# Kernel optimization log

Measured on AMD Instinct MI355X. Metric: run time of the kernel, lower is better.

Reference implementation:

```python
import jax, jax.numpy as jnp
import numpy as np

B, HM_C, H, W = 8, 2, 152, 272
EMB = 128
KOBJ = 128
KGATHER = 8192
NID = (500, 300)
HM_WEIGHT, WH_WEIGHT, OFF_WEIGHT = 1.0, 0.1, 1.0


def setup_inputs() -> dict:
    key = jax.random.key(0)
    ks = jax.random.split(key, 16)
    hm_pred = jax.random.normal(ks[0], (B, HM_C, H, W), jnp.float32)
    wh_pred = jax.random.normal(ks[1], (B, 2, H, W), jnp.float32)
    reg_pred = jax.random.normal(ks[2], (B, 2, H, W), jnp.float32)
    id_pred = jax.random.normal(ks[3], (B, EMB, H, W), jnp.float32)
    ind = jax.random.randint(ks[4], (B, KOBJ), 0, H * W, jnp.int32)
    cls_obj = jax.random.randint(ks[5], (B, KOBJ), 0, HM_C, jnp.int32)
    # gaussian-ish heatmap in [0,1) with exact 1.0 at object centers
    hm = jax.random.uniform(ks[6], (B, HM_C, H, W), jnp.float32) ** 4
    bidx = jnp.arange(B)[:, None]
    hm = hm.reshape(B, HM_C, H * W).at[bidx, cls_obj, ind].set(1.0).reshape(B, HM_C, H, W)
    wh = jax.random.uniform(ks[7], (B, KOBJ, 2), jnp.float32) * 50.0
    reg = jax.random.uniform(ks[8], (B, KOBJ, 2), jnp.float32)
    reg_mask = (jax.random.uniform(ks[9], (B, KOBJ)) < 0.5).astype(jnp.float32)
    u = jax.random.uniform(ks[10], (B, 1, H, W))
    cmap = jax.random.randint(ks[11], (B, 1, H, W), 0, HM_C, jnp.int32)
    cls_id_map = jnp.where(u < 0.01, cmap, -1).astype(jnp.int32)
    cls_tr_ids = jnp.stack([
        jax.random.randint(ks[12], (B, H, W), 0, NID[0], jnp.int32),
        jax.random.randint(ks[13], (B, H, W), 0, NID[1], jnp.int32)], axis=1)
    W0 = jax.random.normal(ks[14], (NID[0], EMB), jnp.float32) * 0.01
    b0 = jnp.zeros((NID[0],), jnp.float32)
    W1 = jax.random.normal(ks[15], (NID[1], EMB), jnp.float32) * 0.01
    b1 = jnp.zeros((NID[1],), jnp.float32)
    s_det = jnp.full((1,), -1.85, jnp.float32)
    s_id = jnp.full((1,), -1.05, jnp.float32)
    return dict(hm_pred=hm_pred, wh_pred=wh_pred, reg_pred=reg_pred, id_pred=id_pred,
                hm=hm, wh=wh, reg=reg, reg_mask=reg_mask, ind=ind,
                cls_id_map=cls_id_map, cls_tr_ids=cls_tr_ids,
                W0=W0, b0=b0, W1=W1, b1=b1, s_det=s_det, s_id=s_id)


def _sigmoid(x):
    return jnp.clip(jax.nn.sigmoid(x), 1e-4, 1.0 - 1e-4)


def focal_loss(pred, gt):
    pos = gt == 1.0
    neg_w = (1.0 - gt) ** 4
    pos_loss = jnp.where(pos, jnp.log(pred) * (1.0 - pred) ** 2, 0.0).sum()
    neg_loss = jnp.where(pos, 0.0, jnp.log(1.0 - pred) * pred ** 2 * neg_w).sum()
    num_pos = pos.sum().astype(pred.dtype)
    return jnp.where(num_pos > 0, -(pos_loss + neg_loss) / jnp.maximum(num_pos, 1.0), -neg_loss)


def gather_feat(feat, ind):  # feat [B,C,H,W], ind [B,K] -> [B,K,C]
    b, c, h, w = feat.shape
    f = feat.reshape(b, c, h * w)
    idx = jnp.broadcast_to(ind[:, None, :], (b, c, ind.shape[1]))
    return jnp.take_along_axis(f, idx, axis=2).transpose(0, 2, 1)


def reg_l1_loss(output, mask, ind, target):
    pred = gather_feat(output, ind)            # [B,K,C]
    m = mask[:, :, None]                       # expanded mask
    c = pred.shape[-1]
    num = jnp.abs(pred * m - target * m).sum()
    return num / (mask.sum() * c + 1e-4)


def reid_class_loss(id_pred, cls_id_map, cls_tr_ids, cls_id, Wc, bc, nid):
    mask = (cls_id_map[:, 0] == cls_id).reshape(-1)              # [B*H*W]
    cnt = mask.sum()
    idx = jnp.nonzero(mask, size=KGATHER, fill_value=0)[0]       # static-size gather
    valid = jnp.arange(KGATHER) < cnt
    feat = id_pred.transpose(0, 2, 3, 1).reshape(-1, EMB)[idx]   # [K,EMB]
    norm = jnp.maximum(jnp.linalg.norm(feat, axis=1, keepdims=True), 1e-12)
    emb_scale = np.float32(np.sqrt(2.0) * np.log(nid - 1.0))
    emb = emb_scale * feat / norm
    logits = emb @ Wc.T + bc                                     # [K,nid]
    tgt = cls_tr_ids[:, cls_id].reshape(-1)[idx]
    tgt = jnp.where(valid, tgt, -1)                              # padded -> ignore_index
    logp = jax.nn.log_softmax(logits, axis=-1)
    nll = jnp.where(tgt >= 0,
                    -jnp.take_along_axis(logp, jnp.clip(tgt, 0)[:, None], axis=1)[:, 0], 0.0)
    n_valid = (tgt >= 0).sum().astype(logits.dtype)
    ce = nll.sum() / jnp.maximum(n_valid, 1.0)                   # CE mean over non-ignored
    term = ce / jnp.maximum(cnt.astype(logits.dtype), 1.0)       # / nelement()
    return jnp.where(cnt > 0, term, 0.0)


def reference(hm_pred, wh_pred, reg_pred, id_pred, hm, wh, reg, reg_mask, ind,
              cls_id_map, cls_tr_ids, W0, b0, W1, b1, s_det, s_id):
    hm_loss = focal_loss(_sigmoid(hm_pred), hm)
    wh_loss = reg_l1_loss(wh_pred, reg_mask, ind, wh)
    off_loss = reg_l1_loss(reg_pred, reg_mask, ind, reg)
    reid_loss = (reid_class_loss(id_pred, cls_id_map, cls_tr_ids, 0, W0, b0, NID[0])
                 + reid_class_loss(id_pred, cls_id_map, cls_tr_ids, 1, W1, b1, NID[1]))
    det_loss = HM_WEIGHT * hm_loss + WH_WEIGHT * wh_loss + OFF_WEIGHT * off_loss
    loss = 0.5 * (jnp.exp(-s_det[0]) * det_loss + jnp.exp(-s_id[0]) * reid_loss
                  + s_det[0] + s_id[0])
    return loss, hm_loss, wh_loss, off_loss, reid_loss
```

## Files before the change

### kernel.cpp

```cpp
#include <hip/hip_runtime.h>
#include <math.h>

#define BB    8
#define HMC   2
#define HW    41344
#define EMBD  128
#define KOBJ  128
#define KG    8192
#define NID0  500
#define NID1  300
#define TE    16


__device__ __forceinline__ float wave_sum(float v) {
    #pragma unroll
    for (int o = 32; o > 0; o >>= 1) v += __shfl_down(v, o, 64);
    return v;
}

__global__ void fused1_kernel(const float4* __restrict__ hp,
                              const float4* __restrict__ gt,
                              const int4*   __restrict__ cmap,
                              const float*  __restrict__ wh_pred,
                              const float*  __restrict__ reg_pred,
                              const float*  __restrict__ wh,
                              const float*  __restrict__ reg,
                              const float*  __restrict__ mask,
                              const int*    __restrict__ ind,
                              float* __restrict__ wsf, int n4, int nc4) {
    int* wsi = (int*)wsf;
    int tid = threadIdx.x;
    int gid = blockIdx.x * blockDim.x + tid;
    int gstride = gridDim.x * blockDim.x;

    __shared__ int stage0[1024], stage1[1024];
    __shared__ int lcnt0, lcnt1, gbase0, gbase1;
    __shared__ float sm[3][4];

    if (tid == 0) { lcnt0 = 0; lcnt1 = 0; }
    __syncthreads();

    for (int i = gid; i < nc4; i += gstride) {
        int4 v = cmap[i];
        int b4 = i * 4;
        if (v.x == 0) stage0[atomicAdd(&lcnt0,1)] = b4+0; else if (v.x == 1) stage1[atomicAdd(&lcnt1,1)] = b4+0;
        if (v.y == 0) stage0[atomicAdd(&lcnt0,1)] = b4+1; else if (v.y == 1) stage1[atomicAdd(&lcnt1,1)] = b4+1;
        if (v.z == 0) stage0[atomicAdd(&lcnt0,1)] = b4+2; else if (v.z == 1) stage1[atomicAdd(&lcnt1,1)] = b4+2;
        if (v.w == 0) stage0[atomicAdd(&lcnt0,1)] = b4+3; else if (v.w == 1) stage1[atomicAdd(&lcnt1,1)] = b4+3;
    }
    __syncthreads();
    if (tid == 0) gbase0 = (lcnt0 > 0) ? atomicAdd(wsi + 8, lcnt0) : 0;
    if (tid == 1) gbase1 = (lcnt1 > 0) ? atomicAdd(wsi + 9, lcnt1) : 0;
    __syncthreads();
    for (int j = tid; j < lcnt0; j += blockDim.x) { int q = gbase0 + j; if (q < KG) wsi[16 + q] = stage0[j]; }
    for (int j = tid; j < lcnt1; j += blockDim.x) { int q = gbase1 + j; if (q < KG) wsi[16 + KG + q] = stage1[j]; }

    float pos = 0.f, neg = 0.f, cnt = 0.f;
    for (int i = gid; i < n4; i += gstride) {
        float4 x = hp[i];
        float4 g = gt[i];
        float xs[4] = {x.x, x.y, x.z, x.w};
        float gs[4] = {g.x, g.y, g.z, g.w};
        #pragma unroll
        for (int j = 0; j < 4; ++j) {
            float s = 1.f / (1.f + expf(-xs[j]));
            s = fminf(fmaxf(s, 1e-4f), 1.f - 1e-4f);
            float gv = gs[j];
            if (gv == 1.f) {
                float om = 1.f - s;
                pos += logf(s) * om * om;
                cnt += 1.f;
            } else {
                float nw = 1.f - gv; nw = nw * nw; nw = nw * nw;
                neg += logf(1.f - s) * s * s * nw;
            }
        }
    }
    {
        float a = wave_sum(pos), b = wave_sum(neg), c = wave_sum(cnt);
        int lane = tid & 63, wid = tid >> 6;
        if (lane == 0) { sm[0][wid] = a; sm[1][wid] = b; sm[2][wid] = c; }
        __syncthreads();
        if (tid == 0) {
            float s0 = 0, s1 = 0, s2 = 0;
            #pragma unroll
            for (int w = 0; w < 4; ++w) { s0 += sm[0][w]; s1 += sm[1][w]; s2 += sm[2][w]; }
            atomicAdd(wsf + 0, s0);
            atomicAdd(wsf + 1, s1);
            atomicAdd(wsf + 2, s2);
        }
    }

    if (blockIdx.x == 0) {
        __syncthreads();
        float nwh = 0.f, noff = 0.f, msum = 0.f;
        for (int t = tid; t < BB * KOBJ; t += blockDim.x) {
            int b = t / KOBJ;
            float m = mask[t];
            int id = ind[t];
            const float* wp = wh_pred + (size_t)b * 2 * HW;
            const float* rp = reg_pred + (size_t)b * 2 * HW;
            float p0 = wp[id], p1 = wp[HW + id];
            float q0 = rp[id], q1 = rp[HW + id];
            float t0 = wh[t * 2], t1 = wh[t * 2 + 1];
            float r0 = reg[t * 2], r1 = reg[t * 2 + 1];
            nwh  += fabsf(p0 * m - t0 * m) + fabsf(p1 * m - t1 * m);
            noff += fabsf(q0 * m - r0 * m) + fabsf(q1 * m - r1 * m);
            msum += m;
        }
        float a = wave_sum(nwh), b = wave_sum(noff), c = wave_sum(msum);
        int lane = tid & 63, wid = tid >> 6;
        if (lane == 0) { sm[0][wid] = a; sm[1][wid] = b; sm[2][wid] = c; }
        __syncthreads();
        if (tid == 0) {
            float s0 = 0, s1 = 0, s2 = 0;
            #pragma unroll
            for (int w = 0; w < 4; ++w) { s0 += sm[0][w]; s1 += sm[1][w]; s2 += sm[2][w]; }
            wsf[3] = s0; wsf[4] = s1; wsf[5] = s2;
        }
    }
}

__global__ void gather_kernel(const float* __restrict__ id_pred,
                              const int*   __restrict__ cls_tr,
                              float* __restrict__ wsf,
                              float esc0, float esc1) {
    int cls = blockIdx.y;
    int* wsi = (int*)wsf;
    int cnt = wsi[8 + cls];
    int m = cnt < KG ? cnt : KG;
    const int* idxArr = wsi + 16 + cls * KG;
    int* tgtArr = wsi + 16 + 2 * KG + cls * KG;
    float* embArr = wsf + 16 + 4 * KG + (size_t)cls * KG * EMBD;
    float escale = cls ? esc1 : esc0;
    __shared__ float red[2];
    int tid = threadIdx.x;
    for (int i = blockIdx.x; i < m; i += gridDim.x) {
        int p = idxArr[i];
        int b = p / HW, hw = p - b * HW;
        float f = id_pred[((size_t)b * EMBD + tid) * HW + hw];
        float ss = f * f;
        #pragma unroll
        for (int o = 32; o > 0; o >>= 1) ss += __shfl_down(ss, o, 64);
        if ((tid & 63) == 0) red[tid >> 6] = ss;
        __syncthreads();
        float s = red[0] + red[1];
        float scale = escale / fmaxf(sqrtf(s), 1e-12f);
        embArr[(size_t)i * EMBD + tid] = f * scale;
        if (tid == 0) tgtArr[i] = cls_tr[((size_t)b * 2 + cls) * HW + hw];
        __syncthreads();
    }
}

__device__ void final_combine(const float* wsf, float nll0, float nll1,
                              int c0, int c1,
                              const float* sdet, const float* sid,
                              float* out) {
    float pos = wsf[0], neg = wsf[1], npos = wsf[2];
    float hm_loss = (npos > 0.f) ? -(pos + neg) / fmaxf(npos, 1.f) : -neg;
    float wh_loss  = wsf[3] / (wsf[5] * 2.f + 1e-4f);
    float off_loss = wsf[4] / (wsf[5] * 2.f + 1e-4f);
    float reid = 0.f;
    if (c0 > 0) {
        float nv = (float)(c0 < KG ? c0 : KG);
        reid += (nll0 / fmaxf(nv, 1.f)) / fmaxf((float)c0, 1.f);
    }
    if (c1 > 0) {
        float nv = (float)(c1 < KG ? c1 : KG);
        reid += (nll1 / fmaxf(nv, 1.f)) / fmaxf((float)c1, 1.f);
    }
    float det = hm_loss + 0.1f * wh_loss + off_loss;
    float sd = sdet[0], si = sid[0];
    out[0] = 0.5f * (expf(-sd) * det + expf(-si) * reid + sd + si);
    out[1] = hm_loss;
    out[2] = wh_loss;
    out[3] = off_loss;
    out[4] = reid;
}

__global__ __launch_bounds__(256)
void reid_logits_kernel(const float* __restrict__ W0, const float* __restrict__ b0,
                        const float* __restrict__ W1, const float* __restrict__ b1,
                        const float* __restrict__ sdet, const float* __restrict__ sid,
                        float* __restrict__ wsf, float* __restrict__ out) {
    int* wsi = (int*)wsf;
    int cls = blockIdx.y;
    int tid = threadIdx.x;

    int c0full = wsi[8], c1full = wsi[9];
    int m0 = c0full < KG ? c0full : KG;
    int m1 = c1full < KG ? c1full : KG;
    int a0 = (m0 + TE - 1) / TE, a1 = (m1 + TE - 1) / TE;
    int nact = a0 + a1;

    if (nact == 0) {
        if (blockIdx.x == 0 && cls == 0 && tid == 0)
            final_combine(wsf, 0.f, 0.f, c0full, c1full, sdet, sid, out);
        return;
    }
    int m = cls ? m1 : m0;
    int base = blockIdx.x * TE;
    if (base >= m) return;
    int nval = m - base; if (nval > TE) nval = TE;

    int nid = cls ? NID1 : NID0;
    const float* Wc = cls ? W1 : W0;
    const float* bc = cls ? b1 : b0;
    const float* embArr = wsf + 16 + 4 * KG + (size_t)cls * KG * EMBD;
    const int*   tgtArr = wsi + 16 + 2 * KG + cls * KG;

    __shared__ float emb_s[TE][EMBD];
    __shared__ int   tgt_s[TE];
    __shared__ float tgtl_s[TE];
    __shared__ float red_m[TE][4];
    __shared__ float red_s[TE][4];

    {
        const float4* src = (const float4*)(embArr + (size_t)base * EMBD);
        float4* dst = (float4*)&emb_s[0][0];
        int lim = nval * (EMBD / 4);
        for (int j = tid; j < TE * (EMBD / 4); j += 256)
            dst[j] = (j < lim) ? src[j] : make_float4(0.f, 0.f, 0.f, 0.f);
    }
    if (tid < TE) { tgt_s[tid] = (tid < nval) ? tgtArr[base + tid] : -1; tgtl_s[tid] = 0.f; }
    __syncthreads();

    int r0 = tid, r1 = tid + 256;
    bool v1ok = r1 < nid;
    const float4* wr0 = (const float4*)(Wc + (size_t)r0 * EMBD);
    const float4* wr1 = (const float4*)(Wc + (size_t)(v1ok ? r1 : 0) * EMBD);

    float acc0[TE], acc1[TE];
    #pragma unroll
    for (int e = 0; e < TE; ++e) { acc0[e] = 0.f; acc1[e] = 0.f; }

    for (int j = 0; j < EMBD / 4; ++j) {
        float4 w0 = wr0[j];
        float4 w1 = wr1[j];
        #pragma unroll
        for (int e = 0; e < TE; ++e) {
            float4 em = ((const float4*)emb_s[e])[j];
            acc0[e] = fmaf(w0.x, em.x, fmaf(w0.y, em.y, fmaf(w0.z, em.z, fmaf(w0.w, em.w, acc0[e]))));
            acc1[e] = fmaf(w1.x, em.x, fmaf(w1.y, em.y, fmaf(w1.z, em.z, fmaf(w1.w, em.w, acc1[e]))));
        }
    }
    float bias0 = bc[r0];
    float bias1 = v1ok ? bc[r1] : 0.f;
    #pragma unroll
    for (int e = 0; e < TE; ++e) {
        acc0[e] += bias0;
        acc1[e] = v1ok ? (acc1[e] + bias1) : -1e30f;
        if (r0 == tgt_s[e]) tgtl_s[e] = acc0[e];
        if (v1ok && r1 == tgt_s[e]) tgtl_s[e] = acc1[e];
    }

    int lane = tid & 63, wid = tid >> 6;

    float mx[TE];
    #pragma unroll
    for (int e = 0; e < TE; ++e) mx[e] = fmaxf(acc0[e], acc1[e]);
    #pragma unroll
    for (int o = 32; o > 0; o >>= 1) {
        #pragma unroll
        for (int e = 0; e < TE; ++e) mx[e] = fmaxf(mx[e], __shfl_xor(mx[e], o, 64));
    }
    if (lane == 0) {
        #pragma unroll
        for (int e = 0; e < TE; ++e) red_m[e][wid] = mx[e];
    }
    __syncthreads();
    float bm[TE];
    #pragma unroll
    for (int e = 0; e < TE; ++e)
        bm[e] = fmaxf(fmaxf(red_m[e][0], red_m[e][1]), fmaxf(red_m[e][2], red_m[e][3]));

    float se[TE];
    #pragma unroll
    for (int e = 0; e < TE; ++e) se[e] = expf(acc0[e] - bm[e]) + expf(acc1[e] - bm[e]);
    #pragma unroll
    for (int o = 32; o > 0; o >>= 1) {
        #pragma unroll
        for (int e = 0; e < TE; ++e) se[e] += __shfl_xor(se[e], o, 64);
    }
    if (lane == 0) {
        #pragma unroll
        for (int e = 0; e < TE; ++e) red_s[e][wid] = se[e];
    }
    __syncthreads();

    if (tid == 0) {
        float nll = 0.f;
        #pragma unroll
        for (int e = 0; e < TE; ++e) {
            if (e < nval) {
                float S = red_s[e][0] + red_s[e][1] + red_s[e][2] + red_s[e][3];
                nll += bm[e] + logf(S) - tgtl_s[e];
            }
        }
        atomicAdd(wsf + 6 + cls, nll);
        __threadfence();
        int old = atomicAdd(wsi + 10, 1);
        if (old == nact - 1) {
            float nll0 = atomicAdd(wsf + 6, 0.f);
            float nll1 = atomicAdd(wsf + 7, 0.f);
            final_combine(wsf, nll0, nll1, c0full, c1full, sdet, sid, out);
        }
    }
}

extern "C" void kernel_launch(void* const* d_in, const int* in_sizes, int n_in,
                              void* d_out, int out_size, void* d_ws, size_t ws_size,
                              hipStream_t stream) {
    const float* hm_pred   = (const float*)d_in[0];
    const float* wh_pred   = (const float*)d_in[1];
    const float* reg_pred  = (const float*)d_in[2];
    const float* id_pred   = (const float*)d_in[3];
    const float* hm        = (const float*)d_in[4];
    const float* wh        = (const float*)d_in[5];
    const float* reg       = (const float*)d_in[6];
    const float* reg_mask  = (const float*)d_in[7];
    const int*   ind       = (const int*)d_in[8];
    const int*   cls_map   = (const int*)d_in[9];
    const int*   cls_tr    = (const int*)d_in[10];
    const float* W0        = (const float*)d_in[11];
    const float* b0        = (const float*)d_in[12];
    const float* W1        = (const float*)d_in[13];
    const float* b1        = (const float*)d_in[14];
    const float* s_det     = (const float*)d_in[15];
    const float* s_id      = (const float*)d_in[16];

    float* wsf = (float*)d_ws;

    hipMemsetAsync(d_ws, 0, 64, stream);

    const int n4  = (BB * HMC * HW) / 4;
    const int nc4 = (BB * HW) / 4;

    fused1_kernel<<<512, 256, 0, stream>>>(
        (const float4*)hm_pred, (const float4*)hm, (const int4*)cls_map,
        wh_pred, reg_pred, wh, reg, reg_mask, ind, wsf, n4, nc4);

    const float esc0 = (float)(sqrt(2.0) * log((double)NID0 - 1.0));
    const float esc1 = (float)(sqrt(2.0) * log((double)NID1 - 1.0));

    gather_kernel<<<dim3(1024, 2), 128, 0, stream>>>(id_pred, cls_tr, wsf, esc0, esc1);

    reid_logits_kernel<<<dim3(KG / TE, 2), 256, 0, stream>>>(
        W0, b0, W1, b1, s_det, s_id, wsf, (float*)d_out);
}
```

Baseline: 87.12 us.

## Fuse three kernels into one persistent kernel with a grid barrier

```diff
diff --git a/kernel.cpp b/kernel.cpp
--- a/kernel.cpp
+++ b/kernel.cpp
@@ -10,6 +10,7 @@
 #define NID0  500
 #define NID1  300
 #define TE    16
+#define GRID  512
 
 
 __device__ __forceinline__ float wave_sum(float v) {
@@ -17,25 +18,64 @@
     for (int o = 32; o > 0; o >>= 1) v += __shfl_down(v, o, 64);
     return v;
 }
-
-__global__ void fused1_kernel(const float4* __restrict__ hp,
-                              const float4* __restrict__ gt,
-                              const int4*   __restrict__ cmap,
-                              const float*  __restrict__ wh_pred,
-                              const float*  __restrict__ reg_pred,
-                              const float*  __restrict__ wh,
-                              const float*  __restrict__ reg,
-                              const float*  __restrict__ mask,
-                              const int*    __restrict__ ind,
-                              float* __restrict__ wsf, int n4, int nc4) {
+__device__ __forceinline__ float aread_f(float* p) { return atomicAdd(p, 0.0f); }
+__device__ __forceinline__ int   aread_i(int* p)   { return atomicAdd(p, 0); }
+
+__device__ void final_combine(float* wsf, int c0, int c1,
+                              const float* sdet, const float* sid,
+                              float* out) {
+    int* wsi = (int*)wsf;
+    (void)wsi;
+    float pos  = aread_f(wsf + 0), neg = aread_f(wsf + 1), npos = aread_f(wsf + 2);
+    float swh  = aread_f(wsf + 3), soff = aread_f(wsf + 4), msum = aread_f(wsf + 5);
+    float nll0 = aread_f(wsf + 6), nll1 = aread_f(wsf + 7);
+    float hm_loss = (npos > 0.f) ? -(pos + neg) / fmaxf(npos, 1.f) : -neg;
+    float wh_loss  = swh  / (msum * 2.f + 1e-4f);
+    float off_loss = soff / (msum * 2.f + 1e-4f);
+    float reid = 0.f;
+    if (c0 > 0) {
+        float nv = (float)(c0 < KG ? c0 : KG);
+        reid += (nll0 / fmaxf(nv, 1.f)) / fmaxf((float)c0, 1.f);
+    }
+    if (c1 > 0) {
+        float nv = (float)(c1 < KG ? c1 : KG);
+        reid += (nll1 / fmaxf(nv, 1.f)) / fmaxf((float)c1, 1.f);
+    }
+    float det = hm_loss + 0.1f * wh_loss + off_loss;
+    float sd = sdet[0], si = sid[0];
+    out[0] = 0.5f * (__expf(-sd) * det + __expf(-si) * reid + sd + si);
+    out[1] = hm_loss;
+    out[2] = wh_loss;
+    out[3] = off_loss;
+    out[4] = reid;
+}
+
+__global__ __launch_bounds__(256, 2)
+void mega_kernel(const float4* __restrict__ hp, const float4* __restrict__ gt,
+                 const int4* __restrict__ cmap,
+                 const float* __restrict__ wh_pred, const float* __restrict__ reg_pred,
+                 const float* __restrict__ wh, const float* __restrict__ reg,
+                 const float* __restrict__ mask, const int* __restrict__ ind,
+                 const float* __restrict__ id_pred, const int* __restrict__ cls_tr,
+                 const float* __restrict__ W0, const float* __restrict__ b0,
+                 const float* __restrict__ W1, const float* __restrict__ b1,
+                 const float* __restrict__ sdet, const float* __restrict__ sid,
+                 float* __restrict__ wsf, float* __restrict__ out,
+                 float esc0, float esc1, int n4, int nc4)
+{
     int* wsi = (int*)wsf;
     int tid = threadIdx.x;
-    int gid = blockIdx.x * blockDim.x + tid;
-    int gstride = gridDim.x * blockDim.x;
+    int gid = blockIdx.x * 256 + tid;
+    const int gstride = GRID * 256;
 
     __shared__ int stage0[1024], stage1[1024];
     __shared__ int lcnt0, lcnt1, gbase0, gbase1;
     __shared__ float sm[3][4];
+    __shared__ float emb_s[TE][EMBD];
+    __shared__ int   tgt_s[TE];
+    __shared__ float tgtl_s[TE];
+    __shared__ float red_m[TE][4];
+    __shared__ float red_s[TE][4];
 
     if (tid == 0) { lcnt0 = 0; lcnt1 = 0; }
     __syncthreads();
@@ -52,31 +92,31 @@
     if (tid == 0) gbase0 = (lcnt0 > 0) ? atomicAdd(wsi + 8, lcnt0) : 0;
     if (tid == 1) gbase1 = (lcnt1 > 0) ? atomicAdd(wsi + 9, lcnt1) : 0;
     __syncthreads();
-    for (int j = tid; j < lcnt0; j += blockDim.x) { int q = gbase0 + j; if (q < KG) wsi[16 + q] = stage0[j]; }
-    for (int j = tid; j < lcnt1; j += blockDim.x) { int q = gbase1 + j; if (q < KG) wsi[16 + KG + q] = stage1[j]; }
-
-    float pos = 0.f, neg = 0.f, cnt = 0.f;
-    for (int i = gid; i < n4; i += gstride) {
-        float4 x = hp[i];
-        float4 g = gt[i];
-        float xs[4] = {x.x, x.y, x.z, x.w};
-        float gs[4] = {g.x, g.y, g.z, g.w};
-        #pragma unroll
-        for (int j = 0; j < 4; ++j) {
-            float s = 1.f / (1.f + expf(-xs[j]));
-            s = fminf(fmaxf(s, 1e-4f), 1.f - 1e-4f);
-            float gv = gs[j];
-            if (gv == 1.f) {
-                float om = 1.f - s;
-                pos += logf(s) * om * om;
-                cnt += 1.f;
-            } else {
-                float nw = 1.f - gv; nw = nw * nw; nw = nw * nw;
-                neg += logf(1.f - s) * s * s * nw;
+    for (int j = tid; j < lcnt0; j += 256) { int q = gbase0 + j; if (q < KG) wsi[16 + q] = stage0[j]; }
+    for (int j = tid; j < lcnt1; j += 256) { int q = gbase1 + j; if (q < KG) wsi[16 + KG + q] = stage1[j]; }
+
+    {
+        float pos = 0.f, neg = 0.f, cnt = 0.f;
+        for (int i = gid; i < n4; i += gstride) {
+            float4 x = hp[i];
+            float4 g = gt[i];
+            float xs[4] = {x.x, x.y, x.z, x.w};
+            float gs[4] = {g.x, g.y, g.z, g.w};
+            #pragma unroll
+            for (int j = 0; j < 4; ++j) {
+                float s = 1.f / (1.f + __expf(-xs[j]));
+                s = fminf(fmaxf(s, 1e-4f), 1.f - 1e-4f);
+                float gv = gs[j];
+                if (gv == 1.f) {
+                    float om = 1.f - s;
+                    pos += __logf(s) * om * om;
+                    cnt += 1.f;
+                } else {
+                    float nw = 1.f - gv; nw = nw * nw; nw = nw * nw;
+                    neg += __logf(1.f - s) * s * s * nw;
+                }
             }
         }
-    }
-    {
         float a = wave_sum(pos), b = wave_sum(neg), c = wave_sum(cnt);
         int lane = tid & 63, wid = tid >> 6;
         if (lane == 0) { sm[0][wid] = a; sm[1][wid] = b; sm[2][wid] = c; }
@@ -94,7 +134,7 @@
     if (blockIdx.x == 0) {
         __syncthreads();
         float nwh = 0.f, noff = 0.f, msum = 0.f;
-        for (int t = tid; t < BB * KOBJ; t += blockDim.x) {
+        for (int t = tid; t < BB * KOBJ; t += 256) {
             int b = t / KOBJ;
             float m = mask[t];
             int id = ind[t];
@@ -116,113 +156,82 @@
             float s0 = 0, s1 = 0, s2 = 0;
             #pragma unroll
             for (int w = 0; w < 4; ++w) { s0 += sm[0][w]; s1 += sm[1][w]; s2 += sm[2][w]; }
-            wsf[3] = s0; wsf[4] = s1; wsf[5] = s2;
-        }
-    }
-}
-
-__global__ void gather_kernel(const float* __restrict__ id_pred,
-                              const int*   __restrict__ cls_tr,
-                              float* __restrict__ wsf,
-                              float esc0, float esc1) {
-    int cls = blockIdx.y;
-    int* wsi = (int*)wsf;
-    int cnt = wsi[8 + cls];
-    int m = cnt < KG ? cnt : KG;
-    const int* idxArr = wsi + 16 + cls * KG;
-    int* tgtArr = wsi + 16 + 2 * KG + cls * KG;
-    float* embArr = wsf + 16 + 4 * KG + (size_t)cls * KG * EMBD;
-    float escale = cls ? esc1 : esc0;
-    __shared__ float red[2];
-    int tid = threadIdx.x;
-    for (int i = blockIdx.x; i < m; i += gridDim.x) {
-        int p = idxArr[i];
-        int b = p / HW, hw = p - b * HW;
-        float f = id_pred[((size_t)b * EMBD + tid) * HW + hw];
-        float ss = f * f;
-        #pragma unroll
-        for (int o = 32; o > 0; o >>= 1) ss += __shfl_down(ss, o, 64);
-        if ((tid & 63) == 0) red[tid >> 6] = ss;
-        __syncthreads();
-        float s = red[0] + red[1];
-        float scale = escale / fmaxf(sqrtf(s), 1e-12f);
-        embArr[(size_t)i * EMBD + tid] = f * scale;
-        if (tid == 0) tgtArr[i] = cls_tr[((size_t)b * 2 + cls) * HW + hw];
-        __syncthreads();
-    }
-}
-
-__device__ void final_combine(const float* wsf, float nll0, float nll1,
-                              int c0, int c1,
-                              const float* sdet, const float* sid,
-                              float* out) {
-    float pos = wsf[0], neg = wsf[1], npos = wsf[2];
-    float hm_loss = (npos > 0.f) ? -(pos + neg) / fmaxf(npos, 1.f) : -neg;
-    float wh_loss  = wsf[3] / (wsf[5] * 2.f + 1e-4f);
-    float off_loss = wsf[4] / (wsf[5] * 2.f + 1e-4f);
-    float reid = 0.f;
-    if (c0 > 0) {
-        float nv = (float)(c0 < KG ? c0 : KG);
-        reid += (nll0 / fmaxf(nv, 1.f)) / fmaxf((float)c0, 1.f);
-    }
-    if (c1 > 0) {
-        float nv = (float)(c1 < KG ? c1 : KG);
-        reid += (nll1 / fmaxf(nv, 1.f)) / fmaxf((float)c1, 1.f);
-    }
-    float det = hm_loss + 0.1f * wh_loss + off_loss;
-    float sd = sdet[0], si = sid[0];
-    out[0] = 0.5f * (expf(-sd) * det + expf(-si) * reid + sd + si);
-    out[1] = hm_loss;
-    out[2] = wh_loss;
-    out[3] = off_loss;
-    out[4] = reid;
-}
-
-__global__ __launch_bounds__(256)
-void reid_logits_kernel(const float* __restrict__ W0, const float* __restrict__ b0,
-                        const float* __restrict__ W1, const float* __restrict__ b1,
-                        const float* __restrict__ sdet, const float* __restrict__ sid,
-                        float* __restrict__ wsf, float* __restrict__ out) {
-    int* wsi = (int*)wsf;
-    int cls = blockIdx.y;
-    int tid = threadIdx.x;
-
-    int c0full = wsi[8], c1full = wsi[9];
+            atomicAdd(wsf + 3, s0);
+            atomicAdd(wsf + 4, s1);
+            atomicAdd(wsf + 5, s2);
+        }
+    }
+
+    __threadfence();
+    __syncthreads();
+    if (tid == 0) {
+        atomicAdd(wsi + 11, 1);
+        while (aread_i(wsi + 11) < GRID) __builtin_amdgcn_s_sleep(8);
+    }
+    __syncthreads();
+
+    int c0full = aread_i(wsi + 8);
+    int c1full = aread_i(wsi + 9);
     int m0 = c0full < KG ? c0full : KG;
     int m1 = c1full < KG ? c1full : KG;
     int a0 = (m0 + TE - 1) / TE, a1 = (m1 + TE - 1) / TE;
     int nact = a0 + a1;
 
     if (nact == 0) {
-        if (blockIdx.x == 0 && cls == 0 && tid == 0)
-            final_combine(wsf, 0.f, 0.f, c0full, c1full, sdet, sid, out);
+        if (blockIdx.x == 0 && tid == 0)
+            final_combine(wsf, c0full, c1full, sdet, sid, out);
         return;
     }
-    int m = cls ? m1 : m0;
-    int base = blockIdx.x * TE;
-    if (base >= m) return;
+    int t = blockIdx.x;
+    if (t >= nact) return;
+    int cls  = (t < a0) ? 0 : 1;
+    int tile = (t < a0) ? t : t - a0;
+    int m    = cls ? m1 : m0;
+    int base = tile * TE;
     int nval = m - base; if (nval > TE) nval = TE;
 
     int nid = cls ? NID1 : NID0;
     const float* Wc = cls ? W1 : W0;
     const float* bc = cls ? b1 : b0;
-    const float* embArr = wsf + 16 + 4 * KG + (size_t)cls * KG * EMBD;
-    const int*   tgtArr = wsi + 16 + 2 * KG + cls * KG;
-
-    __shared__ float emb_s[TE][EMBD];
-    __shared__ int   tgt_s[TE];
-    __shared__ float tgtl_s[TE];
-    __shared__ float red_m[TE][4];
-    __shared__ float red_s[TE][4];
+    int* idxArr = wsi + 16 + cls * KG;
+    float escale = cls ? esc1 : esc0;
 
     {
-        const float4* src = (const float4*)(embArr + (size_t)base * EMBD);
-        float4* dst = (float4*)&emb_s[0][0];
-        int lim = nval * (EMBD / 4);
-        for (int j = tid; j < TE * (EMBD / 4); j += 256)
-            dst[j] = (j < lim) ? src[j] : make_float4(0.f, 0.f, 0.f, 0.f);
-    }
-    if (tid < TE) { tgt_s[tid] = (tid < nval) ? tgtArr[base + tid] : -1; tgtl_s[tid] = 0.f; }
+        int e  = tid >> 4;
+        int cg = tid & 15;
+        if (e < nval) {
+            int p = aread_i(idxArr + base + e);
+            int b = p / HW, hw = p - b * HW;
+            const float* src = id_pred + (size_t)b * EMBD * HW + hw;
+            float f[8];
+            float ss = 0.f;
+            #pragma unroll
+            for (int j = 0; j < 8; ++j) {
+                f[j] = src[(size_t)(cg * 8 + j) * HW];
+                ss += f[j] * f[j];
+            }
+            #pragma unroll
+            for (int o = 1; o < 16; o <<= 1) ss += __shfl_xor(ss, o, 64);
+            float scale = escale / fmaxf(__builtin_sqrtf(ss), 1e-12f);
+            float4* dst = (float4*)&emb_s[e][cg * 8];
+            dst[0] = make_float4(f[0]*scale, f[1]*scale, f[2]*scale, f[3]*scale);
+            dst[1] = make_float4(f[4]*scale, f[5]*scale, f[6]*scale, f[7]*scale);
+        } else {
+            float4* dst = (float4*)&emb_s[e][cg * 8];
+            dst[0] = make_float4(0.f, 0.f, 0.f, 0.f);
+            dst[1] = make_float4(0.f, 0.f, 0.f, 0.f);
+        }
+        if (tid < TE) {
+            int tg = -1;
+            if (tid < nval) {
+                int p = aread_i(idxArr + base + tid);
+                int b = p / HW, hw = p - b * HW;
+                tg = cls_tr[((size_t)b * 2 + cls) * HW + hw];
+            }
+            tgt_s[tid] = tg;
+            tgtl_s[tid] = 0.f;
+        }
+    }
     __syncthreads();
 
     int r0 = tid, r1 = tid + 256;
@@ -276,7 +285,7 @@
 
     float se[TE];
     #pragma unroll
-    for (int e = 0; e < TE; ++e) se[e] = expf(acc0[e] - bm[e]) + expf(acc1[e] - bm[e]);
+    for (int e = 0; e < TE; ++e) se[e] = __expf(acc0[e] - bm[e]) + __expf(acc1[e] - bm[e]);
     #pragma unroll
     for (int o = 32; o > 0; o >>= 1) {
         #pragma unroll
@@ -294,17 +303,14 @@
         for (int e = 0; e < TE; ++e) {
             if (e < nval) {
                 float S = red_s[e][0] + red_s[e][1] + red_s[e][2] + red_s[e][3];
-                nll += bm[e] + logf(S) - tgtl_s[e];
+                nll += bm[e] + __logf(S) - tgtl_s[e];
             }
         }
         atomicAdd(wsf + 6 + cls, nll);
         __threadfence();
         int old = atomicAdd(wsi + 10, 1);
-        if (old == nact - 1) {
-            float nll0 = atomicAdd(wsf + 6, 0.f);
-            float nll1 = atomicAdd(wsf + 7, 0.f);
-            final_combine(wsf, nll0, nll1, c0full, c1full, sdet, sid, out);
-        }
+        if (old == nact - 1)
+            final_combine(wsf, c0full, c1full, sdet, sid, out);
     }
 }
 
@@ -335,16 +341,12 @@
 
     const int n4  = (BB * HMC * HW) / 4;
     const int nc4 = (BB * HW) / 4;
-
-    fused1_kernel<<<512, 256, 0, stream>>>(
-        (const float4*)hm_pred, (const float4*)hm, (const int4*)cls_map,
-        wh_pred, reg_pred, wh, reg, reg_mask, ind, wsf, n4, nc4);
-
     const float esc0 = (float)(sqrt(2.0) * log((double)NID0 - 1.0));
     const float esc1 = (float)(sqrt(2.0) * log((double)NID1 - 1.0));
 
-    gather_kernel<<<dim3(1024, 2), 128, 0, stream>>>(id_pred, cls_tr, wsf, esc0, esc1);
-
-    reid_logits_kernel<<<dim3(KG / TE, 2), 256, 0, stream>>>(
-        W0, b0, W1, b1, s_det, s_id, wsf, (float*)d_out);
+    mega_kernel<<<GRID, 256, 0, stream>>>(
+        (const float4*)hm_pred, (const float4*)hm, (const int4*)cls_map,
+        wh_pred, reg_pred, wh, reg, reg_mask, ind,
+        id_pred, cls_tr, W0, b0, W1, b1, s_det, s_id,
+        wsf, (float*)d_out, esc0, esc1, n4, nc4);
 }
```

Result: slower. 130.0 us (+49.3%).

## Fuse embedding gather/normalize into reid logits kernel with 512-thread blocks

Applied to the files above, without the earlier changes.

```diff
diff --git a/kernel.cpp b/kernel.cpp
--- a/kernel.cpp
+++ b/kernel.cpp
@@ -18,16 +18,17 @@
     return v;
 }
 
-__global__ void fused1_kernel(const float4* __restrict__ hp,
-                              const float4* __restrict__ gt,
-                              const int4*   __restrict__ cmap,
-                              const float*  __restrict__ wh_pred,
-                              const float*  __restrict__ reg_pred,
-                              const float*  __restrict__ wh,
-                              const float*  __restrict__ reg,
-                              const float*  __restrict__ mask,
-                              const int*    __restrict__ ind,
-                              float* __restrict__ wsf, int n4, int nc4) {
+__global__ __launch_bounds__(256)
+void fused1_kernel(const float4* __restrict__ hp,
+                   const float4* __restrict__ gt,
+                   const int4*   __restrict__ cmap,
+                   const float*  __restrict__ wh_pred,
+                   const float*  __restrict__ reg_pred,
+                   const float*  __restrict__ wh,
+                   const float*  __restrict__ reg,
+                   const float*  __restrict__ mask,
+                   const int*    __restrict__ ind,
+                   float* __restrict__ wsf, int n4, int nc4) {
     int* wsi = (int*)wsf;
     int tid = threadIdx.x;
     int gid = blockIdx.x * blockDim.x + tid;
@@ -52,31 +53,31 @@
     if (tid == 0) gbase0 = (lcnt0 > 0) ? atomicAdd(wsi + 8, lcnt0) : 0;
     if (tid == 1) gbase1 = (lcnt1 > 0) ? atomicAdd(wsi + 9, lcnt1) : 0;
     __syncthreads();
-    for (int j = tid; j < lcnt0; j += blockDim.x) { int q = gbase0 + j; if (q < KG) wsi[16 + q] = stage0[j]; }
-    for (int j = tid; j < lcnt1; j += blockDim.x) { int q = gbase1 + j; if (q < KG) wsi[16 + KG + q] = stage1[j]; }
-
-    float pos = 0.f, neg = 0.f, cnt = 0.f;
-    for (int i = gid; i < n4; i += gstride) {
-        float4 x = hp[i];
-        float4 g = gt[i];
-        float xs[4] = {x.x, x.y, x.z, x.w};
-        float gs[4] = {g.x, g.y, g.z, g.w};
-        #pragma unroll
-        for (int j = 0; j < 4; ++j) {
-            float s = 1.f / (1.f + expf(-xs[j]));
-            s = fminf(fmaxf(s, 1e-4f), 1.f - 1e-4f);
-            float gv = gs[j];
-            if (gv == 1.f) {
-                float om = 1.f - s;
-                pos += logf(s) * om * om;
-                cnt += 1.f;
-            } else {
-                float nw = 1.f - gv; nw = nw * nw; nw = nw * nw;
-                neg += logf(1.f - s) * s * s * nw;
+    for (int j = tid; j < lcnt0; j += 256) { int q = gbase0 + j; if (q < KG) wsi[16 + q] = stage0[j]; }
+    for (int j = tid; j < lcnt1; j += 256) { int q = gbase1 + j; if (q < KG) wsi[16 + KG + q] = stage1[j]; }
+
+    {
+        float pos = 0.f, neg = 0.f, cnt = 0.f;
+        for (int i = gid; i < n4; i += gstride) {
+            float4 x = hp[i];
+            float4 g = gt[i];
+            float xs[4] = {x.x, x.y, x.z, x.w};
+            float gs[4] = {g.x, g.y, g.z, g.w};
+            #pragma unroll
+            for (int j = 0; j < 4; ++j) {
+                float s = 1.f / (1.f + __expf(-xs[j]));
+                s = fminf(fmaxf(s, 1e-4f), 1.f - 1e-4f);
+                float gv = gs[j];
+                if (gv == 1.f) {
+                    float om = 1.f - s;
+                    pos += __logf(s) * om * om;
+                    cnt += 1.f;
+                } else {
+                    float nw = 1.f - gv; nw = nw * nw; nw = nw * nw;
+                    neg += __logf(1.f - s) * s * s * nw;
+                }
             }
         }
-    }
-    {
         float a = wave_sum(pos), b = wave_sum(neg), c = wave_sum(cnt);
         int lane = tid & 63, wid = tid >> 6;
         if (lane == 0) { sm[0][wid] = a; sm[1][wid] = b; sm[2][wid] = c; }
@@ -94,7 +95,7 @@
     if (blockIdx.x == 0) {
         __syncthreads();
         float nwh = 0.f, noff = 0.f, msum = 0.f;
-        for (int t = tid; t < BB * KOBJ; t += blockDim.x) {
+        for (int t = tid; t < BB * KOBJ; t += 256) {
             int b = t / KOBJ;
             float m = mask[t];
             int id = ind[t];
@@ -121,45 +122,16 @@
     }
 }
 
-__global__ void gather_kernel(const float* __restrict__ id_pred,
-                              const int*   __restrict__ cls_tr,
-                              float* __restrict__ wsf,
-                              float esc0, float esc1) {
-    int cls = blockIdx.y;
-    int* wsi = (int*)wsf;
-    int cnt = wsi[8 + cls];
-    int m = cnt < KG ? cnt : KG;
-    const int* idxArr = wsi + 16 + cls * KG;
-    int* tgtArr = wsi + 16 + 2 * KG + cls * KG;
-    float* embArr = wsf + 16 + 4 * KG + (size_t)cls * KG * EMBD;
-    float escale = cls ? esc1 : esc0;
-    __shared__ float red[2];
-    int tid = threadIdx.x;
-    for (int i = blockIdx.x; i < m; i += gridDim.x) {
-        int p = idxArr[i];
-        int b = p / HW, hw = p - b * HW;
-        float f = id_pred[((size_t)b * EMBD + tid) * HW + hw];
-        float ss = f * f;
-        #pragma unroll
-        for (int o = 32; o > 0; o >>= 1) ss += __shfl_down(ss, o, 64);
-        if ((tid & 63) == 0) red[tid >> 6] = ss;
-        __syncthreads();
-        float s = red[0] + red[1];
-        float scale = escale / fmaxf(sqrtf(s), 1e-12f);
-        embArr[(size_t)i * EMBD + tid] = f * scale;
-        if (tid == 0) tgtArr[i] = cls_tr[((size_t)b * 2 + cls) * HW + hw];
-        __syncthreads();
-    }
-}
-
-__device__ void final_combine(const float* wsf, float nll0, float nll1,
-                              int c0, int c1,
-                              const float* sdet, const float* sid,
+__device__ void final_combine(const float* wsf, const float* sdet, const float* sid,
                               float* out) {
-    float pos = wsf[0], neg = wsf[1], npos = wsf[2];
+    const int* wsi = (const int*)wsf;
+    float pos  = wsf[0], neg = wsf[1], npos = wsf[2];
+    float swh  = wsf[3], soff = wsf[4], msum = wsf[5];
+    float nll0 = wsf[6], nll1 = wsf[7];
+    int c0 = wsi[8], c1 = wsi[9];
     float hm_loss = (npos > 0.f) ? -(pos + neg) / fmaxf(npos, 1.f) : -neg;
-    float wh_loss  = wsf[3] / (wsf[5] * 2.f + 1e-4f);
-    float off_loss = wsf[4] / (wsf[5] * 2.f + 1e-4f);
+    float wh_loss  = swh  / (msum * 2.f + 1e-4f);
+    float off_loss = soff / (msum * 2.f + 1e-4f);
     float reid = 0.f;
     if (c0 > 0) {
         float nv = (float)(c0 < KG ? c0 : KG);
@@ -171,21 +143,24 @@
     }
     float det = hm_loss + 0.1f * wh_loss + off_loss;
     float sd = sdet[0], si = sid[0];
-    out[0] = 0.5f * (expf(-sd) * det + expf(-si) * reid + sd + si);
+    out[0] = 0.5f * (__expf(-sd) * det + __expf(-si) * reid + sd + si);
     out[1] = hm_loss;
     out[2] = wh_loss;
     out[3] = off_loss;
     out[4] = reid;
 }
 
-__global__ __launch_bounds__(256)
-void reid_logits_kernel(const float* __restrict__ W0, const float* __restrict__ b0,
-                        const float* __restrict__ W1, const float* __restrict__ b1,
-                        const float* __restrict__ sdet, const float* __restrict__ sid,
-                        float* __restrict__ wsf, float* __restrict__ out) {
+__global__ __launch_bounds__(512)
+void reid_fused_kernel(const float* __restrict__ id_pred,
+                       const int*   __restrict__ cls_tr,
+                       const float* __restrict__ W0, const float* __restrict__ b0,
+                       const float* __restrict__ W1, const float* __restrict__ b1,
+                       const float* __restrict__ sdet, const float* __restrict__ sid,
+                       float* __restrict__ wsf, float* __restrict__ out,
+                       float esc0, float esc1) {
     int* wsi = (int*)wsf;
+    int tid = threadIdx.x;
     int cls = blockIdx.y;
-    int tid = threadIdx.x;
 
     int c0full = wsi[8], c1full = wsi[9];
     int m0 = c0full < KG ? c0full : KG;
@@ -195,7 +170,7 @@
 
     if (nact == 0) {
         if (blockIdx.x == 0 && cls == 0 && tid == 0)
-            final_combine(wsf, 0.f, 0.f, c0full, c1full, sdet, sid, out);
+            final_combine(wsf, sdet, sid, out);
         return;
     }
     int m = cls ? m1 : m0;
@@ -203,62 +178,78 @@
     if (base >= m) return;
     int nval = m - base; if (nval > TE) nval = TE;
 
-    int nid = cls ? NID1 : NID0;
+    const int nid = cls ? NID1 : NID0;
     const float* Wc = cls ? W1 : W0;
     const float* bc = cls ? b1 : b0;
-    const float* embArr = wsf + 16 + 4 * KG + (size_t)cls * KG * EMBD;
-    const int*   tgtArr = wsi + 16 + 2 * KG + cls * KG;
+    const int* idxArr = wsi + 16 + cls * KG;
+    const float escale = cls ? esc1 : esc0;
 
     __shared__ float emb_s[TE][EMBD];
     __shared__ int   tgt_s[TE];
     __shared__ float tgtl_s[TE];
-    __shared__ float red_m[TE][4];
-    __shared__ float red_s[TE][4];
+    __shared__ float red_m[TE][8];
+    __shared__ float red_s[TE][8];
 
     {
-        const float4* src = (const float4*)(embArr + (size_t)base * EMBD);
-        float4* dst = (float4*)&emb_s[0][0];
-        int lim = nval * (EMBD / 4);
-        for (int j = tid; j < TE * (EMBD / 4); j += 256)
-            dst[j] = (j < lim) ? src[j] : make_float4(0.f, 0.f, 0.f, 0.f);
-    }
-    if (tid < TE) { tgt_s[tid] = (tid < nval) ? tgtArr[base + tid] : -1; tgtl_s[tid] = 0.f; }
-    __syncthreads();
-
-    int r0 = tid, r1 = tid + 256;
-    bool v1ok = r1 < nid;
-    const float4* wr0 = (const float4*)(Wc + (size_t)r0 * EMBD);
-    const float4* wr1 = (const float4*)(Wc + (size_t)(v1ok ? r1 : 0) * EMBD);
-
-    float acc0[TE], acc1[TE];
-    #pragma unroll
-    for (int e = 0; e < TE; ++e) { acc0[e] = 0.f; acc1[e] = 0.f; }
+        int e  = tid >> 5;
+        int cg = tid & 31;
+        if (e < nval) {
+            int p = idxArr[base + e];
+            int b = p / HW, hw = p - b * HW;
+            const float* src = id_pred + (size_t)b * EMBD * HW + hw;
+            float f0 = src[(size_t)(cg * 4 + 0) * HW];
+            float f1 = src[(size_t)(cg * 4 + 1) * HW];
+            float f2 = src[(size_t)(cg * 4 + 2) * HW];
+            float f3 = src[(size_t)(cg * 4 + 3) * HW];
+            float ss = f0*f0 + f1*f1 + f2*f2 + f3*f3;
+            #pragma unroll
+            for (int o = 1; o < 32; o <<= 1) ss += __shfl_xor(ss, o, 64);
+            float scale = escale / fmaxf(__builtin_sqrtf(ss), 1e-12f);
+            *(float4*)&emb_s[e][cg * 4] = make_float4(f0*scale, f1*scale, f2*scale, f3*scale);
+        } else {
+            *(float4*)&emb_s[e][cg * 4] = make_float4(0.f, 0.f, 0.f, 0.f);
+        }
+        if (tid < TE) {
+            int tg = -1;
+            if (tid < nval) {
+                int p = idxArr[base + tid];
+                int b = p / HW, hw = p - b * HW;
+                tg = cls_tr[((size_t)b * 2 + cls) * HW + hw];
+            }
+            tgt_s[tid] = tg;
+            tgtl_s[tid] = 0.f;
+        }
+    }
+    __syncthreads();
+
+    int r = tid;
+    bool rok = r < nid;
+    const float4* wr = (const float4*)(Wc + (size_t)(rok ? r : 0) * EMBD);
+
+    float acc[TE];
+    #pragma unroll
+    for (int e = 0; e < TE; ++e) acc[e] = 0.f;
 
     for (int j = 0; j < EMBD / 4; ++j) {
-        float4 w0 = wr0[j];
-        float4 w1 = wr1[j];
+        float4 w = wr[j];
         #pragma unroll
         for (int e = 0; e < TE; ++e) {
             float4 em = ((const float4*)emb_s[e])[j];
-            acc0[e] = fmaf(w0.x, em.x, fmaf(w0.y, em.y, fmaf(w0.z, em.z, fmaf(w0.w, em.w, acc0[e]))));
-            acc1[e] = fmaf(w1.x, em.x, fmaf(w1.y, em.y, fmaf(w1.z, em.z, fmaf(w1.w, em.w, acc1[e]))));
-        }
-    }
-    float bias0 = bc[r0];
-    float bias1 = v1ok ? bc[r1] : 0.f;
+            acc[e] = fmaf(w.x, em.x, fmaf(w.y, em.y, fmaf(w.z, em.z, fmaf(w.w, em.w, acc[e]))));
+        }
+    }
+    float bias = rok ? bc[r] : 0.f;
     #pragma unroll
     for (int e = 0; e < TE; ++e) {
-        acc0[e] += bias0;
-        acc1[e] = v1ok ? (acc1[e] + bias1) : -1e30f;
-        if (r0 == tgt_s[e]) tgtl_s[e] = acc0[e];
-        if (v1ok && r1 == tgt_s[e]) tgtl_s[e] = acc1[e];
+        acc[e] = rok ? (acc[e] + bias) : -1e30f;
+        if (rok && r == tgt_s[e]) tgtl_s[e] = acc[e];
     }
 
     int lane = tid & 63, wid = tid >> 6;
 
     float mx[TE];
     #pragma unroll
-    for (int e = 0; e < TE; ++e) mx[e] = fmaxf(acc0[e], acc1[e]);
+    for (int e = 0; e < TE; ++e) mx[e] = acc[e];
     #pragma unroll
     for (int o = 32; o > 0; o >>= 1) {
         #pragma unroll
@@ -271,12 +262,17 @@
     __syncthreads();
     float bm[TE];
     #pragma unroll
-    for (int e = 0; e < TE; ++e)
-        bm[e] = fmaxf(fmaxf(red_m[e][0], red_m[e][1]), fmaxf(red_m[e][2], red_m[e][3]));
+    for (int e = 0; e < TE; ++e) {
+        float v0 = fmaxf(red_m[e][0], red_m[e][1]);
+        float v1 = fmaxf(red_m[e][2], red_m[e][3]);
+        float v2 = fmaxf(red_m[e][4], red_m[e][5]);
+        float v3 = fmaxf(red_m[e][6], red_m[e][7]);
+        bm[e] = fmaxf(fmaxf(v0, v1), fmaxf(v2, v3));
+    }
 
     float se[TE];
     #pragma unroll
-    for (int e = 0; e < TE; ++e) se[e] = expf(acc0[e] - bm[e]) + expf(acc1[e] - bm[e]);
+    for (int e = 0; e < TE; ++e) se[e] = __expf(acc[e] - bm[e]);
     #pragma unroll
     for (int o = 32; o > 0; o >>= 1) {
         #pragma unroll
@@ -293,18 +289,16 @@
         #pragma unroll
         for (int e = 0; e < TE; ++e) {
             if (e < nval) {
-                float S = red_s[e][0] + red_s[e][1] + red_s[e][2] + red_s[e][3];
-                nll += bm[e] + logf(S) - tgtl_s[e];
+                float S = red_s[e][0] + red_s[e][1] + red_s[e][2] + red_s[e][3]
+                        + red_s[e][4] + red_s[e][5] + red_s[e][6] + red_s[e][7];
+                nll += bm[e] + __logf(S) - tgtl_s[e];
             }
         }
         atomicAdd(wsf + 6 + cls, nll);
         __threadfence();
         int old = atomicAdd(wsi + 10, 1);
-        if (old == nact - 1) {
-            float nll0 = atomicAdd(wsf + 6, 0.f);
-            float nll1 = atomicAdd(wsf + 7, 0.f);
-            final_combine(wsf, nll0, nll1, c0full, c1full, sdet, sid, out);
-        }
+        if (old == nact - 1)
+            final_combine(wsf, sdet, sid, out);
     }
 }
 
@@ -335,16 +329,14 @@
 
     const int n4  = (BB * HMC * HW) / 4;
     const int nc4 = (BB * HW) / 4;
+    const float esc0 = (float)(sqrt(2.0) * log((double)NID0 - 1.0));
+    const float esc1 = (float)(sqrt(2.0) * log((double)NID1 - 1.0));
 
     fused1_kernel<<<512, 256, 0, stream>>>(
         (const float4*)hm_pred, (const float4*)hm, (const int4*)cls_map,
         wh_pred, reg_pred, wh, reg, reg_mask, ind, wsf, n4, nc4);
 
-    const float esc0 = (float)(sqrt(2.0) * log((double)NID0 - 1.0));
-    const float esc1 = (float)(sqrt(2.0) * log((double)NID1 - 1.0));
-
-    gather_kernel<<<dim3(1024, 2), 128, 0, stream>>>(id_pred, cls_tr, wsf, esc0, esc1);
-
-    reid_logits_kernel<<<dim3(KG / TE, 2), 256, 0, stream>>>(
-        W0, b0, W1, b1, s_det, s_id, wsf, (float*)d_out);
-}
+    reid_fused_kernel<<<dim3(KG / TE, 2), 512, 0, stream>>>(
+        id_pred, cls_tr, W0, b0, W1, b1, s_det, s_id,
+        wsf, (float*)d_out, esc0, esc1);
+}
```

After: 90.42 us. +3.8%, slower.
